# Kernel optimization log

Measured on AMD Instinct MI355X. Metric: run time of the kernel, lower is better.

Reference implementation:

```python
import jax, jax.numpy as jnp
import numpy as np

H, N, CH = 1024, 64, 1
SEQ_L = 2048

def setup_inputs() -> dict:
    key = jax.random.key(0)
    k0, k1, k2, k3, k4 = jax.random.split(key, 5)
    A_real = jax.random.normal(k0, (H, N), jnp.float32) * 0.5      # log(-Re A)
    A_imag = jax.random.normal(k1, (H, N), jnp.float32) * jnp.pi   # Im A
    B = jax.random.normal(k2, (1, H, N, 2), jnp.float32)           # complex as (.., 2)
    C = jax.random.normal(k3, (CH, H, N, 2), jnp.float32)
    inv_dt = jax.random.normal(k4, (H,), jnp.float32) * 0.5 - 4.0  # log(dt), dt ~ 1e-2
    return {"A_real": A_real, "A_imag": A_imag, "B": B, "C": C,
            "inv_dt": inv_dt, "L": SEQ_L}

def reference(A_real, A_imag, B, C, inv_dt, L):
    rate = 1.0
    # process_ssm_params: exp transforms for dt and real part of A
    dt = jnp.exp(inv_dt) * rate                       # (H,)
    A = -jnp.exp(A_real) + 1j * A_imag                # (H, N) complex
    Bc = B[..., 0] + 1j * B[..., 1]                   # (1, H, N)
    Cc = C[..., 0] + 1j * C[..., 1]                   # (CH, H, N)
    dtA = A * dt[:, None]                             # (H, N)
    # C <- (B[:,None] * C).view(-1, H, N)
    Cm = (Bc[:, None, :, :] * Cc).reshape(-1, H, N)   # (CH, H, N)
    # zoh discretization
    Cm = Cm * (jnp.exp(dtA) - 1.0) / A                # (CH, H, N)
    # log-Vandermonde product: K[c,h,l] = 2*Re sum_n Cm[c,h,n] * exp(dtA[h,n]*l)
    t = jnp.arange(L, dtype=jnp.float32)              # (L,)
    vand = jnp.exp(dtA[:, :, None] * t)               # (H, N, L) complex, the big intermediate
    K = 2.0 * jnp.einsum('chn,hnl->chl', Cm, vand).real  # (CH, H, L)
    K = K.reshape(-1, CH, H, L)
    return K[-1]                                      # (CH, H, L), state is None
```

## Files before the change

kernel.cpp:

```cpp
#include <hip/hip_runtime.h>
#include <math.h>


#define HH 1024
#define NN 64
#define TPB 128
#define LPT 16
#define LOG2E  1.4426950408889634f
#define INV2PI 0.15915494309189535f

__global__ __launch_bounds__(TPB) void s4d_recur2_kernel(
    const float* __restrict__ A_real,
    const float* __restrict__ A_imag,
    const float* __restrict__ B,
    const float* __restrict__ C,
    const float* __restrict__ inv_dt,
    float* __restrict__ out,
    int L)
{
    __shared__ float4 pA[NN];
    __shared__ float4 pW[NN];

    const int h = blockIdx.x;
    const int t = threadIdx.x;

    if (t < NN) {
        const int n  = t;
        const int hn = h * NN + n;
        float Ar = A_real[hn];
        float Ai = A_imag[hn];
        float dt = expf(inv_dt[h]);
        float are = -expf(Ar);
        float dre = dt * are;
        float dim = dt * Ai;
        float er = expf(dre);
        float s, c;
        sincosf(dim, &s, &c);
        float em1r = er * c - 1.0f;
        float em1i = er * s;
        float inv = 1.0f / (are * are + Ai * Ai);
        float zr = (em1r * are + em1i * Ai) * inv;
        float zi = (em1i * are - em1r * Ai) * inv;
        float br = B[2 * hn],  bi = B[2 * hn + 1];
        float Cr = C[2 * hn],  Ci = C[2 * hn + 1];
        float bcr = br * Cr - bi * Ci;
        float bci = br * Ci + bi * Cr;
        float cmr = bcr * zr - bci * zi;
        float cmi = bcr * zi + bci * zr;

        float dreL = dre * LOG2E;
        float dimR = dim * INV2PI;
        float we = exp2f(dreL * (float)TPB);
        float wx = dimR * (float)TPB;
        float wf = wx - floorf(wx);
        float Wc = __builtin_amdgcn_cosf(wf);
        float Ws = __builtin_amdgcn_sinf(wf);
        float Wr = we * Wc, Wi = we * Ws;
        pA[n] = make_float4(dreL, dimR, 2.0f * cmr, 2.0f * cmi);
        pW[n] = make_float4(Wr, Wi, 2.0f * Wr, Wr * Wr + Wi * Wi);
    }
    __syncthreads();

    float acc[LPT];
#pragma unroll
    for (int j = 0; j < LPT; ++j) acc[j] = 0.0f;

    const float tf = (float)t;

    for (int n = 0; n < NN; n += 4) {
        float xp[4], xc[4], aa[4], bb[4];
#pragma unroll
        for (int k = 0; k < 4; ++k) {
            const float4 p = pA[n + k];
            const float4 w = pW[n + k];
            float e = __builtin_amdgcn_exp2f(p.x * tf);
            float x = p.y * tf;
            float f = x - floorf(x);
            float c = __builtin_amdgcn_cosf(f);
            float s = __builtin_amdgcn_sinf(f);
            float er = e * c, ei = e * s;
            float sr = p.z * er - p.w * ei;
            float si = p.z * ei + p.w * er;
            xp[k] = sr;
            xc[k] = sr * w.x - si * w.y;
            aa[k] = w.z;
            bb[k] = w.w;
        }
        acc[0] += (xp[0] + xp[1]) + (xp[2] + xp[3]);
#pragma unroll
        for (int j = 1; j < LPT; ++j) {
#pragma unroll
            for (int k = 0; k < 4; ++k) {
                acc[j] += xc[k];
                float xn = fmaf(aa[k], xc[k], -bb[k] * xp[k]);
                xp[k] = xc[k];
                xc[k] = xn;
            }
        }
    }

#pragma unroll
    for (int j = 0; j < LPT; ++j) {
        out[h * L + j * TPB + t] = acc[j];
    }
}

extern "C" void kernel_launch(void* const* d_in, const int* in_sizes, int n_in,
                              void* d_out, int out_size, void* d_ws, size_t ws_size,
                              hipStream_t stream) {
    const float* A_real = (const float*)d_in[0];
    const float* A_imag = (const float*)d_in[1];
    const float* B      = (const float*)d_in[2];
    const float* C      = (const float*)d_in[3];
    const float* inv_dt = (const float*)d_in[4];
    int L = out_size / HH;

    s4d_recur2_kernel<<<HH, TPB, 0, stream>>>(A_real, A_imag, B, C, inv_dt,
                                              (float*)d_out, L);
}
```

Before: 78.94 us.

## Split state dimension across waves with LDS reduction and longer recurrence

Each block now has 256 threads in four waves. Each wave handles 16 of the 64 state modes over 64 positions with a stride-64 recurrence of 32 steps, where before every thread looped over all 64 modes with 16 steps. Partial sums go to padded shared memory and are reduced across waves before a coalesced store. The aim is fewer transcendental evaluations per output and more parallelism per block. The cost is a 33 KB LDS buffer, an extra barrier and reduction pass, and longer recurrences that may lose accuracy.

Measured after the change: 79.34 us. No clear change (+0.5%).

```diff
diff --git a/kernel.cpp b/kernel.cpp
--- a/kernel.cpp
+++ b/kernel.cpp
@@ -4,12 +4,16 @@
 
 #define HH 1024
 #define NN 64
-#define TPB 128
-#define LPT 16
+#define TPB 256
+#define NWAVE 4
+#define NPW 16
+#define STEP 64
+#define LPT 32
+#define RJ 33
 #define LOG2E  1.4426950408889634f
 #define INV2PI 0.15915494309189535f
 
-__global__ __launch_bounds__(TPB) void s4d_recur2_kernel(
+__global__ __launch_bounds__(TPB, 4) void s4d_recur3_kernel(
     const float* __restrict__ A_real,
     const float* __restrict__ A_imag,
     const float* __restrict__ B,
@@ -20,9 +24,12 @@
 {
     __shared__ float4 pA[NN];
     __shared__ float4 pW[NN];
+    __shared__ float red[NWAVE * STEP * RJ];
 
-    const int h = blockIdx.x;
-    const int t = threadIdx.x;
+    const int h    = blockIdx.x;
+    const int t    = threadIdx.x;
+    const int lane = t & 63;
+    const int w    = t >> 6;
 
     if (t < NN) {
         const int n  = t;
@@ -50,8 +57,8 @@
 
         float dreL = dre * LOG2E;
         float dimR = dim * INV2PI;
-        float we = exp2f(dreL * (float)TPB);
-        float wx = dimR * (float)TPB;
+        float we = exp2f(dreL * (float)STEP);
+        float wx = dimR * (float)STEP;
         float wf = wx - floorf(wx);
         float Wc = __builtin_amdgcn_cosf(wf);
         float Ws = __builtin_amdgcn_sinf(wf);
@@ -65,14 +72,15 @@
 #pragma unroll
     for (int j = 0; j < LPT; ++j) acc[j] = 0.0f;
 
-    const float tf = (float)t;
+    const float tf = (float)lane;
+    const int n0 = w * NPW;
 
-    for (int n = 0; n < NN; n += 4) {
+    for (int g = 0; g < NPW; g += 4) {
         float xp[4], xc[4], aa[4], bb[4];
 #pragma unroll
         for (int k = 0; k < 4; ++k) {
-            const float4 p = pA[n + k];
-            const float4 w = pW[n + k];
+            const float4 p = pA[n0 + g + k];
+            const float4 ww = pW[n0 + g + k];
             float e = __builtin_amdgcn_exp2f(p.x * tf);
             float x = p.y * tf;
             float f = x - floorf(x);
@@ -82,9 +90,9 @@
             float sr = p.z * er - p.w * ei;
             float si = p.z * ei + p.w * er;
             xp[k] = sr;
-            xc[k] = sr * w.x - si * w.y;
-            aa[k] = w.z;
-            bb[k] = w.w;
+            xc[k] = sr * ww.x - si * ww.y;
+            aa[k] = ww.z;
+            bb[k] = ww.w;
         }
         acc[0] += (xp[0] + xp[1]) + (xp[2] + xp[3]);
 #pragma unroll
@@ -99,9 +107,23 @@
         }
     }
 
+    {
+        float* dst = &red[(w * STEP + lane) * RJ];
 #pragma unroll
-    for (int j = 0; j < LPT; ++j) {
-        out[h * L + j * TPB + t] = acc[j];
+        for (int j = 0; j < LPT; ++j) dst[j] = acc[j];
+    }
+    __syncthreads();
+
+#pragma unroll
+    for (int r = 0; r < 8; ++r) {
+        int p = t + TPB * r;
+        int j  = p >> 6;
+        int l2 = p & 63;
+        float sum = 0.0f;
+#pragma unroll
+        for (int v = 0; v < NWAVE; ++v)
+            sum += red[(v * STEP + l2) * RJ + j];
+        out[h * L + p] = sum;
     }
 }
 
@@ -115,6 +137,6 @@
     const float* inv_dt = (const float*)d_in[4];
     int L = out_size / HH;
 
-    s4d_recur2_kernel<<<HH, TPB, 0, stream>>>(A_real, A_imag, B, C, inv_dt,
+    s4d_recur3_kernel<<<HH, TPB, 0, stream>>>(A_real, A_imag, B, C, inv_dt,
                                               (float*)d_out, L);
 }
```
